# Kernel tuning notes

Measured on AMD Instinct MI355X. Metric: run time of the kernel, lower is better.

Reference implementation:

```python
import jax, jax.numpy as jnp
import numpy as np

B, N, C = 8, 8192, 256
H = 8            # num_heads
D = C // H       # head dim = 32
P = 64           # proj_size (Linformer rank)


def setup_inputs() -> dict:
    key = jax.random.key(0)
    ks = jax.random.split(key, 12)
    s = lambda fan_in: 1.0 / np.sqrt(fan_in)
    return {
        "x": jax.random.normal(ks[0], (B, N, C), jnp.float32),
        "Wqkvv": jax.random.normal(ks[1], (4 * C, C), jnp.float32) * s(C),
        "WE": jax.random.normal(ks[2], (P, N), jnp.float32) * s(N),
        "bE": jax.random.normal(ks[3], (P,), jnp.float32) * s(N),
        "WF": jax.random.normal(ks[4], (P, N), jnp.float32) * s(N),
        "bF": jax.random.normal(ks[5], (P,), jnp.float32) * s(N),
        "Wo1": jax.random.normal(ks[6], (C // 2, C), jnp.float32) * s(C),
        "bo1": jax.random.normal(ks[7], (C // 2,), jnp.float32) * s(C),
        "Wo2": jax.random.normal(ks[8], (C // 2, C), jnp.float32) * s(C),
        "bo2": jax.random.normal(ks[9], (C // 2,), jnp.float32) * s(C),
        "temp1": jnp.ones((H, 1, 1), jnp.float32),
        "temp2": jnp.ones((H, 1, 1), jnp.float32),
    }


def _l2norm(v, axis=-1, eps=1e-12):
    # matches torch F.normalize
    n = jnp.sqrt(jnp.sum(v * v, axis=axis, keepdims=True))
    return v / jnp.maximum(n, eps)


def reference(x, Wqkvv, WE, bE, WF, bF, Wo1, bo1, Wo2, bo2, temp1, temp2):
    b, n, c = x.shape
    # qkvv: [b,n,4c] -> [4,b,h,d,n]  (includes the .transpose(-2,-1) of each part)
    qkvv = jnp.einsum('bnc,fc->bnf', x, Wqkvv).reshape(b, n, 4, H, D)
    qkvv = qkvv.transpose(2, 0, 3, 4, 1)
    q, k, v_ca, v_sa = qkvv[0], qkvv[1], qkvv[2], qkvv[3]  # each [b,h,d,n]

    # Linformer-style low-rank projections along the token axis
    k_proj = jnp.einsum('bhdn,pn->bhdp', k, WE) + bE   # [b,h,d,p]
    v_proj = jnp.einsum('bhdn,pn->bhdp', v_sa, WF) + bF

    qn = _l2norm(q)
    kn = _l2norm(k)

    # --- channel attention branch (XCiT-style) ---
    attn_ca = jnp.einsum('bhdn,bhen->bhde', qn, kn) * temp1[None]  # [b,h,d,d]
    attn_ca = jax.nn.softmax(attn_ca, axis=-1)  # dropout: eval mode (identity)
    x_ca = jnp.einsum('bhde,bhen->bhdn', attn_ca, v_ca)
    x_ca = x_ca.transpose(0, 3, 1, 2).reshape(b, n, c)  # [b,n,c]

    # --- spatial attention branch (low-rank) ---
    attn_sa = jnp.einsum('bhdn,bhdp->bhnp', qn, k_proj) * temp2[None]  # [b,h,n,p]
    attn_sa = jax.nn.softmax(attn_sa, axis=-1)
    x_sa = jnp.einsum('bhnp,bhdp->bhnd', attn_sa, v_proj)  # [b,h,n,d]
    # faithful to original: permute(0,3,1,2).reshape(b,n,c)
    x_sa = x_sa.transpose(0, 3, 1, 2).reshape(b, n, c)

    x_sa = jnp.einsum('bnc,oc->bno', x_sa, Wo1) + bo1
    x_ca = jnp.einsum('bnc,oc->bno', x_ca, Wo2) + bo2
    return jnp.concatenate((x_sa, x_ca), axis=-1)
```

## Files before the change

### kernel.cpp

```cpp
#include <hip/hip_runtime.h>
#include <hip/hip_bf16.h>
#include <stdint.h>


typedef __attribute__((ext_vector_type(8))) __bf16 bf16x8;
typedef __attribute__((ext_vector_type(4))) __bf16 bf16x4;
typedef __attribute__((ext_vector_type(4))) float f32x4;

#define MFMA(a, b, c) __builtin_amdgcn_mfma_f32_16x16x32_bf16((a), (b), (c), 0, 0, 0)

__device__ __forceinline__ void gl2lds16(const __bf16* g, __bf16* l) {
  __builtin_amdgcn_global_load_lds(
      (const __attribute__((address_space(1))) void*)(const void*)g,
      (__attribute__((address_space(3))) void*)(void*)l, 16, 0, 0);
}

__device__ __forceinline__ int detect_f32(const unsigned int* __restrict__ xw) {
  int c = 0;
#pragma unroll
  for (int i = 0; i < 64; ++i) {
    const unsigned int u = xw[i];
    c += (((u >> 7) & 0xFF) >= 0xC0) ? 1 : 0;
    c += (((u >> 23) & 0xFF) >= 0xC0) ? 1 : 0;
  }
  return c > 8;
}

__global__ __launch_bounds__(256) void k_convert_x(const void* __restrict__ src,
                                                   __bf16* __restrict__ dst) {
  const int i = (blockIdx.x * 256 + threadIdx.x) * 8;
  if (detect_f32((const unsigned int*)src)) {
    const float* s = (const float*)src;
    bf16x8 v;
#pragma unroll
    for (int j = 0; j < 8; ++j) v[j] = (__bf16)s[i + j];
    *(bf16x8*)(dst + i) = v;
  } else {
    *(bf16x8*)(dst + i) = *(const bf16x8*)((const __bf16*)src + i);
  }
}

__global__ __launch_bounds__(256) void k_convert_w(
    const void* s0, const void* s1, const void* s2, const void* s3, const void* s4,
    const void* s5, const void* s6, const void* s7, const void* s8, const void* s9,
    const void* s10, __bf16* __restrict__ cw, const void* __restrict__ xsrc) {
  const int i = (blockIdx.x * 256 + threadIdx.x) * 8;
  if (i >= 1376656) return;
  const void* s;
  int base;
  if (i < 262144)        { s = s0;  base = 0; }
  else if (i < 786432)   { s = s1;  base = 262144; }
  else if (i < 786496)   { s = s2;  base = 786432; }
  else if (i < 1310784)  { s = s3;  base = 786496; }
  else if (i < 1310848)  { s = s4;  base = 1310784; }
  else if (i < 1343616)  { s = s5;  base = 1310848; }
  else if (i < 1343744)  { s = s6;  base = 1343616; }
  else if (i < 1376512)  { s = s7;  base = 1343744; }
  else if (i < 1376640)  { s = s8;  base = 1376512; }
  else if (i < 1376648)  { s = s9;  base = 1376640; }
  else                   { s = s10; base = 1376648; }
  const int li = i - base;
  if (detect_f32((const unsigned int*)xsrc)) {
    const float* sf = (const float*)s;
#pragma unroll
    for (int j = 0; j < 8; ++j) cw[i + j] = (__bf16)sf[li + j];
  } else {
    const __bf16* sb = (const __bf16*)s;
#pragma unroll
    for (int j = 0; j < 8; ++j) cw[i + j] = sb[li + j];
  }
}

__global__ __launch_bounds__(256) void k_qkvv(const __bf16* __restrict__ x,
                                              const __bf16* __restrict__ Wq,
                                              __bf16* __restrict__ qkvv,
                                              float* __restrict__ npart) {
  __shared__ alignas(16) __bf16 As[128 * 32];
  __shared__ alignas(16) __bf16 Bs[128 * 32];
  __shared__ alignas(16) __bf16 Cs[32 * 136];
  const int t = threadIdx.x, lane = t & 63;
  const int wr = t >> 7, wc = (t >> 6) & 1;
  const int l15 = lane & 15, g = lane >> 4;
  const int f0 = blockIdx.y * 128;
  const int t0 = blockIdx.x * 128;
  f32x4 acc[4][4] = {};
  const int r = t >> 2;
  const int c8 = ((t & 3) ^ ((t >> 3) & 3)) * 8;
  const int cx = ((g ^ ((l15 >> 1) & 3)) * 8);
  for (int k0 = 0; k0 < 256; k0 += 32) {
#pragma unroll
    for (int i = 0; i < 2; ++i) {
      gl2lds16(Wq + (size_t)(f0 + i * 64 + r) * 256 + k0 + c8, As + i * 2048 + t * 8);
      gl2lds16(x + (size_t)(t0 + i * 64 + r) * 256 + k0 + c8, Bs + i * 2048 + t * 8);
    }
    __syncthreads();
    bf16x8 af[4], bfr[4];
#pragma unroll
    for (int i = 0; i < 4; ++i) {
      af[i] = *(const bf16x8*)(As + (wr * 64 + i * 16 + l15) * 32 + cx);
      bfr[i] = *(const bf16x8*)(Bs + (wc * 64 + i * 16 + l15) * 32 + cx);
    }
#pragma unroll
    for (int i = 0; i < 4; ++i)
#pragma unroll
      for (int j = 0; j < 4; ++j) acc[i][j] = MFMA(af[i], bfr[j], acc[i][j]);
    __syncthreads();
  }
  const int b = t0 >> 13;
  const int n0 = t0 & 8191;
  for (int i = 0; i < 4; ++i) {
    if (i) __syncthreads();
#pragma unroll
    for (int j = 0; j < 4; ++j)
#pragma unroll
      for (int rr = 0; rr < 4; ++rr)
        Cs[(wr * 16 + g * 4 + rr) * 136 + wc * 64 + j * 16 + l15] = (__bf16)acc[i][j][rr];
    __syncthreads();
#pragma unroll
    for (int half = 0; half < 2; ++half) {
      const int row_l = (t >> 4) + half * 16;
      const int col8 = (t & 15) * 8;
      const bf16x8 v = *(const bf16x8*)(Cs + row_l * 136 + col8);
      const int f = f0 + (row_l >> 4) * 64 + i * 16 + (row_l & 15);
      *(bf16x8*)(qkvv + (size_t)(((f >> 8) * 8 + b) * 256 + (f & 255)) * 8192 + n0 + col8) = v;
      if (f0 < 512) {
        float s = 0.f;
#pragma unroll
        for (int jj = 0; jj < 8; ++jj) { const float q = (float)v[jj]; s += q * q; }
#pragma unroll
        for (int off = 1; off < 16; off <<= 1) s += __shfl_xor(s, off, 16);
        if ((t & 15) == 0) npart[(size_t)blockIdx.x * 512 + f] = s;
      }
    }
  }
}

__global__ __launch_bounds__(256) void k_nred(const float* __restrict__ npart,
                                              float* __restrict__ qsum,
                                              float* __restrict__ ksum) {
  const int which = blockIdx.x >> 3, b = blockIdx.x & 7;
  const int c = threadIdx.x;
  float s = 0.f;
#pragma unroll 4
  for (int j = 0; j < 64; ++j)
    s += npart[(size_t)(b * 64 + j) * 512 + which * 256 + c];
  (which ? ksum : qsum)[b * 256 + c] = s;
}

__global__ __launch_bounds__(256) void k_proj_part(const __bf16* __restrict__ qkvv,
                                                   const __bf16* __restrict__ WE,
                                                   const __bf16* __restrict__ WF,
                                                   float* __restrict__ pbuf) {
  __shared__ alignas(16) __bf16 As[128 * 32];
  __shared__ alignas(16) __bf16 Bs[64 * 32];
  const int t = threadIdx.x, lane = t & 63;
  const int wr = t >> 7, wc = (t >> 6) & 1;
  const int l15 = lane & 15, g = lane >> 4;
  const int kc = blockIdx.x, mt = blockIdx.y, pj = blockIdx.z;
  const __bf16* A = qkvv + (size_t)(pj ? 3 : 1) * 2048 * 8192;
  const __bf16* Bm = pj ? WF : WE;
  const int r0 = mt * 128;
  f32x4 acc[4][2] = {};
  const int r = t >> 2;
  const int c8 = ((t & 3) ^ ((t >> 3) & 3)) * 8;
  const int cx = ((g ^ ((l15 >> 1) & 3)) * 8);
  for (int k0 = kc * 512; k0 < kc * 512 + 512; k0 += 32) {
#pragma unroll
    for (int i = 0; i < 2; ++i)
      gl2lds16(A + (size_t)(r0 + i * 64 + r) * 8192 + k0 + c8, As + i * 2048 + t * 8);
    gl2lds16(Bm + (size_t)r * 8192 + k0 + c8, Bs + t * 8);
    __syncthreads();
    bf16x8 af[4], bfr[2];
#pragma unroll
    for (int i = 0; i < 4; ++i)
      af[i] = *(const bf16x8*)(As + (wr * 64 + i * 16 + l15) * 32 + cx);
#pragma unroll
    for (int j = 0; j < 2; ++j)
      bfr[j] = *(const bf16x8*)(Bs + (wc * 32 + j * 16 + l15) * 32 + cx);
#pragma unroll
    for (int i = 0; i < 4; ++i)
#pragma unroll
      for (int j = 0; j < 2; ++j) acc[i][j] = MFMA(af[i], bfr[j], acc[i][j]);
    __syncthreads();
  }
  float* dst = pbuf + (size_t)((pj * 16 + kc) * 2048 + r0) * 64;
#pragma unroll
  for (int i = 0; i < 4; ++i)
#pragma unroll
    for (int j = 0; j < 2; ++j)
#pragma unroll
      for (int rr = 0; rr < 4; ++rr)
        dst[(wr * 64 + i * 16 + g * 4 + rr) * 64 + wc * 32 + j * 16 + l15] = acc[i][j][rr];
}

__global__ __launch_bounds__(256) void k_proj_reduce(const float* __restrict__ pbuf,
                                                     const __bf16* __restrict__ bE,
                                                     const __bf16* __restrict__ bF,
                                                     const float* __restrict__ qsum,
                                                     const __bf16* __restrict__ t2,
                                                     __bf16* __restrict__ kprojT,
                                                     __bf16* __restrict__ vprojb) {
  const int idx = blockIdx.x * 256 + threadIdx.x;
  const int pj = idx >> 17, rp = idx & 131071, p = idx & 63;
  const int row = rp >> 6, bh = row >> 5, d = row & 31, h = bh & 7;
  float s = (float)((pj ? bF : bE)[p]);
  const float* src = pbuf + (size_t)pj * 16 * 131072 + rp;
#pragma unroll
  for (int k = 0; k < 16; ++k) s += src[(size_t)k * 131072];
  if (pj == 0) {
    const float qi = 1.0f / fmaxf(sqrtf(qsum[row]), 1e-12f);
    kprojT[bh * 2048 + p * 32 + d] = (__bf16)(s * qi * (float)t2[h]);
  } else {
    vprojb[bh * 2048 + d * 64 + p] = (__bf16)s;
  }
}

__global__ __launch_bounds__(256) void k_sca_part(const __bf16* __restrict__ qkvv,
                                                  float* __restrict__ spart) {
  const int bh = blockIdx.x, kc = blockIdx.y;
  const int t = threadIdx.x, lane = t & 63, w = t >> 6;
  const __bf16* qb = qkvv + (size_t)(bh * 32) * 8192;
  const __bf16* kb = qkvv + (size_t)(2048 + bh * 32) * 8192;
  f32x4 acc[2][2] = {};
  const int kbase = kc * 1024 + w * 256 + (lane >> 4) * 8;
#pragma unroll
  for (int ks = 0; ks < 256; ks += 32) {
    bf16x8 af[2], bfr[2];
#pragma unroll
    for (int i = 0; i < 2; ++i) {
      af[i] = *(const bf16x8*)(qb + (size_t)(i * 16 + (lane & 15)) * 8192 + kbase + ks);
      bfr[i] = *(const bf16x8*)(kb + (size_t)(i * 16 + (lane & 15)) * 8192 + kbase + ks);
    }
#pragma unroll
    for (int i = 0; i < 2; ++i)
#pragma unroll
      for (int j = 0; j < 2; ++j) acc[i][j] = MFMA(af[i], bfr[j], acc[i][j]);
  }
  float* dst = spart + (size_t)((bh * 8 + kc) * 4 + w) * 1024;
#pragma unroll
  for (int i = 0; i < 2; ++i)
#pragma unroll
    for (int j = 0; j < 2; ++j)
#pragma unroll
      for (int rr = 0; rr < 4; ++rr)
        dst[(i * 16 + (lane >> 4) * 4 + rr) * 32 + j * 16 + (lane & 15)] = acc[i][j][rr];
}

__global__ __launch_bounds__(256) void k_sca_softmax(const float* __restrict__ spart,
                                                     const float* __restrict__ qsum,
                                                     const float* __restrict__ ksum,
                                                     const __bf16* __restrict__ temp1,
                                                     __bf16* __restrict__ attnb) {
  const int bh = blockIdx.x;
  __shared__ float S[1024];
  const int t = threadIdx.x;
  const float tmp = (float)temp1[bh & 7];
  for (int idx = t; idx < 1024; idx += 256) {
    float s = 0.f;
    const float* src = spart + (size_t)bh * 32768 + idx;
#pragma unroll
    for (int k = 0; k < 32; ++k) s += src[k * 1024];
    const float qi = 1.0f / fmaxf(sqrtf(qsum[bh * 32 + (idx >> 5)]), 1e-12f);
    const float ki = 1.0f / fmaxf(sqrtf(ksum[bh * 32 + (idx & 31)]), 1e-12f);
    S[idx] = s * qi * ki * tmp;
  }
  __syncthreads();
  const int lane = t & 63, w = t >> 6;
#pragma unroll
  for (int rr = 0; rr < 4; ++rr) {
    const int row = rr * 8 + w * 2 + (lane >> 5);
    const int e = lane & 31;
    float v = S[row * 32 + e];
    float m = v;
#pragma unroll
    for (int off = 16; off; off >>= 1) m = fmaxf(m, __shfl_xor(m, off, 32));
    const float ex = __expf(v - m);
    float sm = ex;
#pragma unroll
    for (int off = 16; off; off >>= 1) sm += __shfl_xor(sm, off, 32);
    attnb[(size_t)bh * 1024 + row * 32 + e] = (__bf16)(ex / sm);
  }
}

__global__ __launch_bounds__(256) void k_casa(const __bf16* __restrict__ qkvv,
                                              const __bf16* __restrict__ attnb,
                                              const __bf16* __restrict__ kprojT,
                                              const __bf16* __restrict__ vprojb,
                                              __bf16* __restrict__ xca,
                                              __bf16* __restrict__ xsa) {
  __shared__ __bf16 P[4][16 * 72];
  const int t = threadIdx.x, lane = t & 63, w = t >> 6;
  const int l15 = lane & 15, g = lane >> 4;
  if (blockIdx.y < 64) {
    const int bh = blockIdx.y, b = bh >> 3, h = bh & 7;
    const __bf16* vb = qkvv + (size_t)(4096 + bh * 32) * 8192;
    bf16x8 aa[2];
#pragma unroll
    for (int mi = 0; mi < 2; ++mi)
      aa[mi] = *(const bf16x8*)(attnb + bh * 1024 + (mi * 16 + l15) * 32 + g * 8);
#pragma unroll
    for (int it = 0; it < 4; ++it) {
      const int n = blockIdx.x * 256 + it * 64 + w * 16 + l15;
      union { bf16x8 v; unsigned short u[8]; } bq;
#pragma unroll
      for (int j = 0; j < 8; ++j)
        bq.u[j] = *(const unsigned short*)(vb + (size_t)(g * 8 + j) * 8192 + n);
      f32x4 o[2] = {};
#pragma unroll
      for (int mi = 0; mi < 2; ++mi) o[mi] = MFMA(aa[mi], bq.v, o[mi]);
#pragma unroll
      for (int mi = 0; mi < 2; ++mi) {
        bf16x4 p4;
#pragma unroll
        for (int rr = 0; rr < 4; ++rr) p4[rr] = (__bf16)o[mi][rr];
        *(bf16x4*)(xca + (size_t)(b * 8192 + n) * 256 + h * 32 + mi * 16 + g * 4) = p4;
      }
    }
  } else {
    const int bh = blockIdx.y - 64;
    const __bf16* qb = qkvv + (size_t)(bh * 32) * 8192;
    bf16x8 ka[4], va[2][2];
#pragma unroll
    for (int tile = 0; tile < 4; ++tile)
      ka[tile] = *(const bf16x8*)(kprojT + bh * 2048 + (tile * 16 + l15) * 32 + g * 8);
#pragma unroll
    for (int mi = 0; mi < 2; ++mi)
#pragma unroll
      for (int kh = 0; kh < 2; ++kh)
        va[mi][kh] = *(const bf16x8*)(vprojb + bh * 2048 + (mi * 16 + l15) * 64 + kh * 32 + g * 8);
    __bf16* Pw = &P[w][0];
#pragma unroll
    for (int it = 0; it < 4; ++it) {
      const int n0 = blockIdx.x * 256 + it * 64 + w * 16;
      union { bf16x8 v; unsigned short u[8]; } bq;
#pragma unroll
      for (int j = 0; j < 8; ++j)
        bq.u[j] = *(const unsigned short*)(qb + (size_t)(g * 8 + j) * 8192 + n0 + l15);
      f32x4 st[4];
#pragma unroll
      for (int tile = 0; tile < 4; ++tile) {
        f32x4 z = {};
        st[tile] = MFMA(ka[tile], bq.v, z);
      }
      float m = st[0][0];
#pragma unroll
      for (int tile = 0; tile < 4; ++tile)
#pragma unroll
        for (int rr = 0; rr < 4; ++rr) m = fmaxf(m, st[tile][rr]);
      m = fmaxf(m, __shfl_xor(m, 16, 64));
      m = fmaxf(m, __shfl_xor(m, 32, 64));
      float sum = 0.f;
#pragma unroll
      for (int tile = 0; tile < 4; ++tile) {
        bf16x4 p4;
#pragma unroll
        for (int rr = 0; rr < 4; ++rr) {
          const float ex = __expf(st[tile][rr] - m);
          sum += ex;
          p4[rr] = (__bf16)ex;
        }
        *(bf16x4*)(Pw + l15 * 72 + tile * 16 + g * 4) = p4;
      }
      sum += __shfl_xor(sum, 16, 64);
      sum += __shfl_xor(sum, 32, 64);
      const float inv = 1.0f / sum;
      f32x4 o[2] = {};
#pragma unroll
      for (int kh = 0; kh < 2; ++kh) {
        const bf16x8 pf = *(const bf16x8*)(Pw + l15 * 72 + kh * 32 + g * 8);
#pragma unroll
        for (int mi = 0; mi < 2; ++mi) o[mi] = MFMA(va[mi][kh], pf, o[mi]);
      }
#pragma unroll
      for (int mi = 0; mi < 2; ++mi)
#pragma unroll
        for (int rr = 0; rr < 4; ++rr) {
          const int d = mi * 16 + g * 4 + rr;
          xsa[(size_t)(bh * 32 + d) * 8192 + n0 + l15] = (__bf16)(o[mi][rr] * inv);
        }
    }
  }
}

__global__ __launch_bounds__(256) void k_out(const __bf16* __restrict__ xsa,
                                             const __bf16* __restrict__ xca,
                                             const __bf16* __restrict__ Wo1,
                                             const __bf16* __restrict__ bo1,
                                             const __bf16* __restrict__ Wo2,
                                             const __bf16* __restrict__ bo2,
                                             void* __restrict__ outv,
                                             const void* __restrict__ xsrc) {
  __shared__ alignas(16) __bf16 As[128 * 32];
  __shared__ alignas(16) __bf16 Bs[128 * 32];
  const int t = threadIdx.x, lane = t & 63;
  const int wr = t >> 7, wc = (t >> 6) & 1;
  const int l15 = lane & 15, g = lane >> 4;
  const int nt = blockIdx.x, b = blockIdx.y, br = blockIdx.z;
  const int isf32 = detect_f32((const unsigned int*)xsrc);
  const __bf16* Wo = br ? Wo2 : Wo1;
  const __bf16* bo = br ? bo2 : bo1;
  f32x4 acc[4][4] = {};
  const int r = t >> 2;
  const int c8 = ((t & 3) ^ ((t >> 3) & 3)) * 8;
  const int cx = ((g ^ ((l15 >> 1) & 3)) * 8);
  for (int k0 = 0; k0 < 256; k0 += 32) {
#pragma unroll
    for (int i = 0; i < 2; ++i) {
      const int row = nt * 128 + i * 64 + r;
      const __bf16* ga;
      if (br == 0) {
        ga = xsa + (size_t)((b * 8 + ((row >> 5) & 7)) * 32 + (row >> 8)) * 8192 +
             (row & 31) * 256 + k0 + c8;
      } else {
        ga = xca + (size_t)(b * 8192 + row) * 256 + k0 + c8;
      }
      gl2lds16(ga, As + i * 2048 + t * 8);
      gl2lds16(Wo + (size_t)(i * 64 + r) * 256 + k0 + c8, Bs + i * 2048 + t * 8);
    }
    __syncthreads();
    bf16x8 af[4], bfr[4];
#pragma unroll
    for (int i = 0; i < 4; ++i) {
      af[i] = *(const bf16x8*)(As + (wr * 64 + i * 16 + l15) * 32 + cx);
      bfr[i] = *(const bf16x8*)(Bs + (wc * 64 + i * 16 + l15) * 32 + cx);
    }
#pragma unroll
    for (int i = 0; i < 4; ++i)
#pragma unroll
      for (int j = 0; j < 4; ++j) acc[i][j] = MFMA(af[i], bfr[j], acc[i][j]);
    __syncthreads();
  }
  float bias[4];
#pragma unroll
  for (int j = 0; j < 4; ++j) bias[j] = (float)bo[wc * 64 + j * 16 + l15];
#pragma unroll
  for (int i = 0; i < 4; ++i) {
#pragma unroll
    for (int j = 0; j < 4; ++j) {
      const int col = wc * 64 + j * 16 + l15;
#pragma unroll
      for (int rr = 0; rr < 4; ++rr) {
        const int row = nt * 128 + wr * 64 + i * 16 + g * 4 + rr;
        const float val = acc[i][j][rr] + bias[j];
        const size_t oi = (size_t)(b * 8192 + row) * 256 + br * 128 + col;
        if (isf32) ((float*)outv)[oi] = val;
        else ((__bf16*)outv)[oi] = (__bf16)val;
      }
    }
  }
}

extern "C" void kernel_launch(void* const* d_in, const int* in_sizes, int n_in,
                              void* d_out, int out_size, void* d_ws, size_t ws_size,
                              hipStream_t stream) {
  char* ws = (char*)d_ws;
  __bf16* qkvv   = (__bf16*)(ws);
  __bf16* cinx   = (__bf16*)(ws + 134217728ull);
  __bf16* xca    = (__bf16*)(ws + 134217728ull);
  float*  pbuf   = (float*)(ws + 167772160ull);
  float*  npart  = (float*)(ws + 184549376ull);
  float*  spart  = (float*)(ws + 184549376ull);
  __bf16* xsa    = (__bf16*)(ws + 167772160ull);
  __bf16* kprojT = (__bf16*)(ws + 201326592ull);
  __bf16* vprojb = (__bf16*)(ws + 201588736ull);
  float*  qsum   = (float*)(ws + 201850880ull);
  float*  ksum   = (float*)(ws + 201859072ull);
  __bf16* attnb  = (__bf16*)(ws + 201867264ull);
  __bf16* cw     = (__bf16*)(ws + 201998336ull);

  __bf16* cWq  = cw;
  __bf16* cWE  = cw + 262144;
  __bf16* cbE  = cw + 786432;
  __bf16* cWF  = cw + 786496;
  __bf16* cbF  = cw + 1310784;
  __bf16* cWo1 = cw + 1310848;
  __bf16* cbo1 = cw + 1343616;
  __bf16* cWo2 = cw + 1343744;
  __bf16* cbo2 = cw + 1376512;
  __bf16* ct1  = cw + 1376640;
  __bf16* ct2  = cw + 1376648;

  k_convert_x<<<8192, 256, 0, stream>>>(d_in[0], cinx);
  k_convert_w<<<673, 256, 0, stream>>>(d_in[1], d_in[2], d_in[3], d_in[4], d_in[5],
                                       d_in[6], d_in[7], d_in[8], d_in[9], d_in[10],
                                       d_in[11], cw, d_in[0]);
  k_qkvv<<<dim3(512, 8), 256, 0, stream>>>(cinx, cWq, qkvv, npart);
  k_nred<<<16, 256, 0, stream>>>(npart, qsum, ksum);
  k_proj_part<<<dim3(16, 16, 2), 256, 0, stream>>>(qkvv, cWE, cWF, pbuf);
  k_proj_reduce<<<dim3(1024), 256, 0, stream>>>(pbuf, cbE, cbF, qsum, ct2, kprojT, vprojb);
  k_sca_part<<<dim3(64, 8), 256, 0, stream>>>(qkvv, spart);
  k_sca_softmax<<<dim3(64), 256, 0, stream>>>(spart, qsum, ksum, ct1, attnb);
  k_casa<<<dim3(32, 128), 256, 0, stream>>>(qkvv, attnb, kprojT, vprojb, xca, xsa);
  k_out<<<dim3(64, 8, 2), 256, 0, stream>>>(xsa, xca, cWo1, cbo1, cWo2, cbo2, d_out, d_in[0]);
}
```

Before: 310.5 us.

## Fuse x conversion into QKVV GEMM with full-K LDS-resident token tile

Drops the separate x-to-bf16 conversion kernel and converts x while loading it into LDS inside the QKVV GEMM. Each block now keeps a 64-token x tile with full K resident in swizzled LDS and computes all 1024 output features, reading the weight fragments straight from global memory or cache without LDS staging. The aim is to remove the x round-trip through memory and the extra launch, and to read x only once instead of once per feature tile. In exchange the weights are re-read by every block, and the norm partials grow to 128 per batch, so the reduction loop changes to match.

```diff
diff --git a/kernel.cpp b/kernel.cpp
--- a/kernel.cpp
+++ b/kernel.cpp
@@ -24,20 +24,6 @@
     c += (((u >> 23) & 0xFF) >= 0xC0) ? 1 : 0;
   }
   return c > 8;
-}
-
-__global__ __launch_bounds__(256) void k_convert_x(const void* __restrict__ src,
-                                                   __bf16* __restrict__ dst) {
-  const int i = (blockIdx.x * 256 + threadIdx.x) * 8;
-  if (detect_f32((const unsigned int*)src)) {
-    const float* s = (const float*)src;
-    bf16x8 v;
-#pragma unroll
-    for (int j = 0; j < 8; ++j) v[j] = (__bf16)s[i + j];
-    *(bf16x8*)(dst + i) = v;
-  } else {
-    *(bf16x8*)(dst + i) = *(const bf16x8*)((const __bf16*)src + i);
-  }
 }
 
 __global__ __launch_bounds__(256) void k_convert_w(
@@ -71,66 +57,81 @@
   }
 }
 
-__global__ __launch_bounds__(256) void k_qkvv(const __bf16* __restrict__ x,
-                                              const __bf16* __restrict__ Wq,
-                                              __bf16* __restrict__ qkvv,
-                                              float* __restrict__ npart) {
-  __shared__ alignas(16) __bf16 As[128 * 32];
-  __shared__ alignas(16) __bf16 Bs[128 * 32];
-  __shared__ alignas(16) __bf16 Cs[32 * 136];
-  const int t = threadIdx.x, lane = t & 63;
-  const int wr = t >> 7, wc = (t >> 6) & 1;
+__global__ __launch_bounds__(256, 3) void k_qkvv(const void* __restrict__ xsrc,
+                                                 const __bf16* __restrict__ Wq,
+                                                 __bf16* __restrict__ qkvv,
+                                                 float* __restrict__ npart) {
+  __shared__ alignas(16) __bf16 Xs[64 * 256];
+  __shared__ alignas(16) __bf16 Csw[4][16][72];
+  const int t = threadIdx.x;
+  const int tile = blockIdx.x;
+  const int b = tile >> 7;
+  const int n0 = (tile & 127) * 64;
+  const int r = t >> 2, q4 = t & 3;
+  if (detect_f32((const unsigned int*)xsrc)) {
+    const float* xf = (const float*)xsrc + (size_t)(b * 8192 + n0 + r) * 256;
+#pragma unroll
+    for (int p = 0; p < 8; ++p) {
+      const int c = q4 + p * 4;
+      const f32x4 a = *(const f32x4*)(xf + c * 8);
+      const f32x4 a2 = *(const f32x4*)(xf + c * 8 + 4);
+      bf16x8 v;
+#pragma unroll
+      for (int j = 0; j < 4; ++j) { v[j] = (__bf16)a[j]; v[4 + j] = (__bf16)a2[j]; }
+      *(bf16x8*)(Xs + r * 256 + ((c ^ (r & 7)) * 8)) = v;
+    }
+  } else {
+    const __bf16* xb = (const __bf16*)xsrc + (size_t)(b * 8192 + n0 + r) * 256;
+#pragma unroll
+    for (int p = 0; p < 8; ++p) {
+      const int c = q4 + p * 4;
+      *(bf16x8*)(Xs + r * 256 + ((c ^ (r & 7)) * 8)) = *(const bf16x8*)(xb + c * 8);
+    }
+  }
+  __syncthreads();
+  const int lane = t & 63, w = t >> 6;
   const int l15 = lane & 15, g = lane >> 4;
-  const int f0 = blockIdx.y * 128;
-  const int t0 = blockIdx.x * 128;
-  f32x4 acc[4][4] = {};
-  const int r = t >> 2;
-  const int c8 = ((t & 3) ^ ((t >> 3) & 3)) * 8;
-  const int cx = ((g ^ ((l15 >> 1) & 3)) * 8);
-  for (int k0 = 0; k0 < 256; k0 += 32) {
-#pragma unroll
-    for (int i = 0; i < 2; ++i) {
-      gl2lds16(Wq + (size_t)(f0 + i * 64 + r) * 256 + k0 + c8, As + i * 2048 + t * 8);
-      gl2lds16(x + (size_t)(t0 + i * 64 + r) * 256 + k0 + c8, Bs + i * 2048 + t * 8);
-    }
-    __syncthreads();
-    bf16x8 af[4], bfr[4];
+  const int sw = l15 & 7;
+  for (int ft = 0; ft < 4; ++ft) {
+    const int f1 = w * 256 + ft * 64;
+    f32x4 acc[4][4] = {};
+#pragma unroll
+    for (int k0 = 0; k0 < 256; k0 += 32) {
+      bf16x8 af[4], bfr[4];
+#pragma unroll
+      for (int i = 0; i < 4; ++i)
+        af[i] = *(const bf16x8*)(Wq + (size_t)(f1 + i * 16 + l15) * 256 + k0 + g * 8);
+#pragma unroll
+      for (int j = 0; j < 4; ++j)
+        bfr[j] = *(const bf16x8*)(Xs + (j * 16 + l15) * 256 + ((((k0 >> 3) + g) ^ sw) * 8));
+#pragma unroll
+      for (int i = 0; i < 4; ++i)
+#pragma unroll
+        for (int j = 0; j < 4; ++j) acc[i][j] = MFMA(af[i], bfr[j], acc[i][j]);
+    }
 #pragma unroll
     for (int i = 0; i < 4; ++i) {
-      af[i] = *(const bf16x8*)(As + (wr * 64 + i * 16 + l15) * 32 + cx);
-      bfr[i] = *(const bf16x8*)(Bs + (wc * 64 + i * 16 + l15) * 32 + cx);
-    }
-#pragma unroll
-    for (int i = 0; i < 4; ++i)
-#pragma unroll
-      for (int j = 0; j < 4; ++j) acc[i][j] = MFMA(af[i], bfr[j], acc[i][j]);
-    __syncthreads();
-  }
-  const int b = t0 >> 13;
-  const int n0 = t0 & 8191;
-  for (int i = 0; i < 4; ++i) {
-    if (i) __syncthreads();
-#pragma unroll
-    for (int j = 0; j < 4; ++j)
-#pragma unroll
-      for (int rr = 0; rr < 4; ++rr)
-        Cs[(wr * 16 + g * 4 + rr) * 136 + wc * 64 + j * 16 + l15] = (__bf16)acc[i][j][rr];
-    __syncthreads();
-#pragma unroll
-    for (int half = 0; half < 2; ++half) {
-      const int row_l = (t >> 4) + half * 16;
-      const int col8 = (t & 15) * 8;
-      const bf16x8 v = *(const bf16x8*)(Cs + row_l * 136 + col8);
-      const int f = f0 + (row_l >> 4) * 64 + i * 16 + (row_l & 15);
-      *(bf16x8*)(qkvv + (size_t)(((f >> 8) * 8 + b) * 256 + (f & 255)) * 8192 + n0 + col8) = v;
-      if (f0 < 512) {
-        float s = 0.f;
-#pragma unroll
-        for (int jj = 0; jj < 8; ++jj) { const float q = (float)v[jj]; s += q * q; }
-#pragma unroll
-        for (int off = 1; off < 16; off <<= 1) s += __shfl_xor(s, off, 16);
-        if ((t & 15) == 0) npart[(size_t)blockIdx.x * 512 + f] = s;
-      }
+      if (f1 < 512) {
+#pragma unroll
+        for (int rr = 0; rr < 4; ++rr) {
+          float s = 0.f;
+#pragma unroll
+          for (int j = 0; j < 4; ++j) { const float v = acc[i][j][rr]; s += v * v; }
+#pragma unroll
+          for (int off = 1; off < 16; off <<= 1) s += __shfl_xor(s, off, 16);
+          if (l15 == 0) npart[(size_t)tile * 512 + f1 + i * 16 + g * 4 + rr] = s;
+        }
+      }
+#pragma unroll
+      for (int j = 0; j < 4; ++j)
+#pragma unroll
+        for (int rr = 0; rr < 4; ++rr)
+          Csw[w][g * 4 + rr][j * 16 + l15] = (__bf16)acc[i][j][rr];
+      const int f = f1 + i * 16 + l15;
+      __bf16* dst = qkvv + (size_t)(((f >> 8) * 8 + b) * 256 + (f & 255)) * 8192 + n0;
+#pragma unroll
+      for (int h = 0; h < 2; ++h)
+        *(bf16x8*)(dst + (h * 4 + g) * 8) = *(const bf16x8*)(&Csw[w][l15][(h * 4 + g) * 8]);
     }
   }
 }
@@ -142,8 +143,8 @@
   const int c = threadIdx.x;
   float s = 0.f;
 #pragma unroll 4
-  for (int j = 0; j < 64; ++j)
-    s += npart[(size_t)(b * 64 + j) * 512 + which * 256 + c];
+  for (int j = 0; j < 128; ++j)
+    s += npart[(size_t)(b * 128 + j) * 512 + which * 256 + c];
   (which ? ksum : qsum)[b * 256 + c] = s;
 }
 
@@ -455,7 +456,6 @@
                               hipStream_t stream) {
   char* ws = (char*)d_ws;
   __bf16* qkvv   = (__bf16*)(ws);
-  __bf16* cinx   = (__bf16*)(ws + 134217728ull);
   __bf16* xca    = (__bf16*)(ws + 134217728ull);
   float*  pbuf   = (float*)(ws + 167772160ull);
   float*  npart  = (float*)(ws + 184549376ull);
@@ -480,11 +480,10 @@
   __bf16* ct1  = cw + 1376640;
   __bf16* ct2  = cw + 1376648;
 
-  k_convert_x<<<8192, 256, 0, stream>>>(d_in[0], cinx);
   k_convert_w<<<673, 256, 0, stream>>>(d_in[1], d_in[2], d_in[3], d_in[4], d_in[5],
                                        d_in[6], d_in[7], d_in[8], d_in[9], d_in[10],
                                        d_in[11], cw, d_in[0]);
-  k_qkvv<<<dim3(512, 8), 256, 0, stream>>>(cinx, cWq, qkvv, npart);
+  k_qkvv<<<dim3(1024), 256, 0, stream>>>(d_in[0], cWq, qkvv, npart);
   k_nred<<<16, 256, 0, stream>>>(npart, qsum, ksum);
   k_proj_part<<<dim3(16, 16, 2), 256, 0, stream>>>(qkvv, cWE, cWF, pbuf);
   k_proj_reduce<<<dim3(1024), 256, 0, stream>>>(pbuf, cbE, cbF, qsum, ct2, kprojT, vprojb);
```

New measurement: 340.8 us. 1.1x slower.

## Fuse x fp32-to-bf16 conversion into QKVV GEMM with double-buffered LDS

Applied to the files above, without the earlier changes.

Removes the standalone k_convert_x kernel. k_qkvv now reads the fp32 input directly, converts it to bf16 in registers and writes it to LDS, which avoids writing and re-reading a 32MB bf16 copy of x. The GEMM K-loop becomes double-buffered so the next K tile's loads overlap the current MFMAs. The grid is transposed so consecutive blocks share the same token tile across feature tiles, which should improve L2 reuse of x. In exchange, LDS use doubles and each block pays a per-block detect_f32 check.

```diff
diff --git a/kernel.cpp b/kernel.cpp
--- a/kernel.cpp
+++ b/kernel.cpp
@@ -24,20 +24,6 @@
     c += (((u >> 23) & 0xFF) >= 0xC0) ? 1 : 0;
   }
   return c > 8;
-}
-
-__global__ __launch_bounds__(256) void k_convert_x(const void* __restrict__ src,
-                                                   __bf16* __restrict__ dst) {
-  const int i = (blockIdx.x * 256 + threadIdx.x) * 8;
-  if (detect_f32((const unsigned int*)src)) {
-    const float* s = (const float*)src;
-    bf16x8 v;
-#pragma unroll
-    for (int j = 0; j < 8; ++j) v[j] = (__bf16)s[i + j];
-    *(bf16x8*)(dst + i) = v;
-  } else {
-    *(bf16x8*)(dst + i) = *(const bf16x8*)((const __bf16*)src + i);
-  }
 }
 
 __global__ __launch_bounds__(256) void k_convert_w(
@@ -71,41 +57,90 @@
   }
 }
 
-__global__ __launch_bounds__(256) void k_qkvv(const __bf16* __restrict__ x,
+__global__ __launch_bounds__(256) void k_qkvv(const void* __restrict__ xsrc,
                                               const __bf16* __restrict__ Wq,
                                               __bf16* __restrict__ qkvv,
                                               float* __restrict__ npart) {
-  __shared__ alignas(16) __bf16 As[128 * 32];
-  __shared__ alignas(16) __bf16 Bs[128 * 32];
+  __shared__ alignas(16) __bf16 As[2][128 * 32];
+  __shared__ alignas(16) __bf16 Bs[2][128 * 32];
   __shared__ alignas(16) __bf16 Cs[32 * 136];
   const int t = threadIdx.x, lane = t & 63;
   const int wr = t >> 7, wc = (t >> 6) & 1;
   const int l15 = lane & 15, g = lane >> 4;
-  const int f0 = blockIdx.y * 128;
-  const int t0 = blockIdx.x * 128;
+  const int f0 = blockIdx.x * 128;
+  const int t0 = blockIdx.y * 128;
+  const int isf32 = detect_f32((const unsigned int*)xsrc);
+  const float* xf = (const float*)xsrc;
+  const __bf16* xb = (const __bf16*)xsrc;
   f32x4 acc[4][4] = {};
   const int r = t >> 2;
   const int c8 = ((t & 3) ^ ((t >> 3) & 3)) * 8;
   const int cx = ((g ^ ((l15 >> 1) & 3)) * 8);
-  for (int k0 = 0; k0 < 256; k0 += 32) {
+
+  if (isf32) {
 #pragma unroll
     for (int i = 0; i < 2; ++i) {
-      gl2lds16(Wq + (size_t)(f0 + i * 64 + r) * 256 + k0 + c8, As + i * 2048 + t * 8);
-      gl2lds16(x + (size_t)(t0 + i * 64 + r) * 256 + k0 + c8, Bs + i * 2048 + t * 8);
+      gl2lds16(Wq + (size_t)(f0 + i * 64 + r) * 256 + c8, &As[0][i * 2048 + t * 8]);
+      const float* src = xf + (size_t)(t0 + i * 64 + r) * 256 + c8;
+      const f32x4 a = *(const f32x4*)src;
+      const f32x4 a2 = *(const f32x4*)(src + 4);
+      bf16x8 v;
+#pragma unroll
+      for (int j = 0; j < 4; ++j) { v[j] = (__bf16)a[j]; v[4 + j] = (__bf16)a2[j]; }
+      *(bf16x8*)(&Bs[0][i * 2048 + t * 8]) = v;
+    }
+  } else {
+#pragma unroll
+    for (int i = 0; i < 2; ++i) {
+      gl2lds16(Wq + (size_t)(f0 + i * 64 + r) * 256 + c8, &As[0][i * 2048 + t * 8]);
+      gl2lds16(xb + (size_t)(t0 + i * 64 + r) * 256 + c8, &Bs[0][i * 2048 + t * 8]);
+    }
+  }
+  __syncthreads();
+
+  for (int ks = 0; ks < 8; ++ks) {
+    const int cur = ks & 1, nxt = cur ^ 1;
+    const int k1 = (ks + 1) * 32;
+    f32x4 a[2], a2[2];
+    if (ks < 7) {
+#pragma unroll
+      for (int i = 0; i < 2; ++i)
+        gl2lds16(Wq + (size_t)(f0 + i * 64 + r) * 256 + k1 + c8, &As[nxt][i * 2048 + t * 8]);
+      if (isf32) {
+#pragma unroll
+        for (int i = 0; i < 2; ++i) {
+          const float* src = xf + (size_t)(t0 + i * 64 + r) * 256 + k1 + c8;
+          a[i] = *(const f32x4*)src;
+          a2[i] = *(const f32x4*)(src + 4);
+        }
+      } else {
+#pragma unroll
+        for (int i = 0; i < 2; ++i)
+          gl2lds16(xb + (size_t)(t0 + i * 64 + r) * 256 + k1 + c8, &Bs[nxt][i * 2048 + t * 8]);
+      }
+    }
+    bf16x8 af[4], bfr[4];
+#pragma unroll
+    for (int i = 0; i < 4; ++i) {
+      af[i] = *(const bf16x8*)(&As[cur][(wr * 64 + i * 16 + l15) * 32 + cx]);
+      bfr[i] = *(const bf16x8*)(&Bs[cur][(wc * 64 + i * 16 + l15) * 32 + cx]);
+    }
+#pragma unroll
+    for (int i = 0; i < 4; ++i)
+#pragma unroll
+      for (int j = 0; j < 4; ++j) acc[i][j] = MFMA(af[i], bfr[j], acc[i][j]);
+    if (ks < 7 && isf32) {
+#pragma unroll
+      for (int i = 0; i < 2; ++i) {
+        bf16x8 v;
+#pragma unroll
+        for (int j = 0; j < 4; ++j) { v[j] = (__bf16)a[i][j]; v[4 + j] = (__bf16)a2[i][j]; }
+        *(bf16x8*)(&Bs[nxt][i * 2048 + t * 8]) = v;
+      }
     }
     __syncthreads();
-    bf16x8 af[4], bfr[4];
-#pragma unroll
-    for (int i = 0; i < 4; ++i) {
-      af[i] = *(const bf16x8*)(As + (wr * 64 + i * 16 + l15) * 32 + cx);
-      bfr[i] = *(const bf16x8*)(Bs + (wc * 64 + i * 16 + l15) * 32 + cx);
-    }
-#pragma unroll
-    for (int i = 0; i < 4; ++i)
-#pragma unroll
-      for (int j = 0; j < 4; ++j) acc[i][j] = MFMA(af[i], bfr[j], acc[i][j]);
-    __syncthreads();
-  }
+  }
+
   const int b = t0 >> 13;
   const int n0 = t0 & 8191;
   for (int i = 0; i < 4; ++i) {
@@ -129,7 +164,7 @@
         for (int jj = 0; jj < 8; ++jj) { const float q = (float)v[jj]; s += q * q; }
 #pragma unroll
         for (int off = 1; off < 16; off <<= 1) s += __shfl_xor(s, off, 16);
-        if ((t & 15) == 0) npart[(size_t)blockIdx.x * 512 + f] = s;
+        if ((t & 15) == 0) npart[(size_t)blockIdx.y * 512 + f] = s;
       }
     }
   }
@@ -455,7 +490,6 @@
                               hipStream_t stream) {
   char* ws = (char*)d_ws;
   __bf16* qkvv   = (__bf16*)(ws);
-  __bf16* cinx   = (__bf16*)(ws + 134217728ull);
   __bf16* xca    = (__bf16*)(ws + 134217728ull);
   float*  pbuf   = (float*)(ws + 167772160ull);
   float*  npart  = (float*)(ws + 184549376ull);
@@ -480,11 +514,10 @@
   __bf16* ct1  = cw + 1376640;
   __bf16* ct2  = cw + 1376648;
 
-  k_convert_x<<<8192, 256, 0, stream>>>(d_in[0], cinx);
   k_convert_w<<<673, 256, 0, stream>>>(d_in[1], d_in[2], d_in[3], d_in[4], d_in[5],
                                        d_in[6], d_in[7], d_in[8], d_in[9], d_in[10],
                                        d_in[11], cw, d_in[0]);
-  k_qkvv<<<dim3(512, 8), 256, 0, stream>>>(cinx, cWq, qkvv, npart);
+  k_qkvv<<<dim3(8, 512), 256, 0, stream>>>(d_in[0], cWq, qkvv, npart);
   k_nred<<<16, 256, 0, stream>>>(npart, qsum, ksum);
   k_proj_part<<<dim3(16, 16, 2), 256, 0, stream>>>(qkvv, cWE, cWF, pbuf);
   k_proj_reduce<<<dim3(1024), 256, 0, stream>>>(pbuf, cbE, cbF, qsum, ct2, kprojT, vprojb);
```

Result: slower. 335.6 us (+8.1%).

## Double-buffer LDS tiles in the qkvv, projection and output GEMM kernels

Applied to the files above, without the earlier changes.

Adds two LDS buffers per operand in three MFMA GEMM kernels. The next k-slice is issued with global_load_lds before computing on the current slice, so memory latency can overlap with MFMA work. LDS use per block doubles, which may lower occupancy, and correctness depends on the trailing __syncthreads covering the async loads.

```diff
diff --git a/kernel.cpp b/kernel.cpp
--- a/kernel.cpp
+++ b/kernel.cpp
@@ -75,8 +75,8 @@
                                               const __bf16* __restrict__ Wq,
                                               __bf16* __restrict__ qkvv,
                                               float* __restrict__ npart) {
-  __shared__ alignas(16) __bf16 As[128 * 32];
-  __shared__ alignas(16) __bf16 Bs[128 * 32];
+  __shared__ alignas(16) __bf16 As[2][128 * 32];
+  __shared__ alignas(16) __bf16 Bs[2][128 * 32];
   __shared__ alignas(16) __bf16 Cs[32 * 136];
   const int t = threadIdx.x, lane = t & 63;
   const int wr = t >> 7, wc = (t >> 6) & 1;
@@ -87,18 +87,27 @@
   const int r = t >> 2;
   const int c8 = ((t & 3) ^ ((t >> 3) & 3)) * 8;
   const int cx = ((g ^ ((l15 >> 1) & 3)) * 8);
-  for (int k0 = 0; k0 < 256; k0 += 32) {
-#pragma unroll
-    for (int i = 0; i < 2; ++i) {
-      gl2lds16(Wq + (size_t)(f0 + i * 64 + r) * 256 + k0 + c8, As + i * 2048 + t * 8);
-      gl2lds16(x + (size_t)(t0 + i * 64 + r) * 256 + k0 + c8, Bs + i * 2048 + t * 8);
-    }
-    __syncthreads();
+#pragma unroll
+  for (int i = 0; i < 2; ++i) {
+    gl2lds16(Wq + (size_t)(f0 + i * 64 + r) * 256 + c8, &As[0][i * 2048 + t * 8]);
+    gl2lds16(x + (size_t)(t0 + i * 64 + r) * 256 + c8, &Bs[0][i * 2048 + t * 8]);
+  }
+  __syncthreads();
+  for (int ks = 0; ks < 8; ++ks) {
+    const int cur = ks & 1, nxt = cur ^ 1;
+    if (ks < 7) {
+      const int k1 = (ks + 1) * 32;
+#pragma unroll
+      for (int i = 0; i < 2; ++i) {
+        gl2lds16(Wq + (size_t)(f0 + i * 64 + r) * 256 + k1 + c8, &As[nxt][i * 2048 + t * 8]);
+        gl2lds16(x + (size_t)(t0 + i * 64 + r) * 256 + k1 + c8, &Bs[nxt][i * 2048 + t * 8]);
+      }
+    }
     bf16x8 af[4], bfr[4];
 #pragma unroll
     for (int i = 0; i < 4; ++i) {
-      af[i] = *(const bf16x8*)(As + (wr * 64 + i * 16 + l15) * 32 + cx);
-      bfr[i] = *(const bf16x8*)(Bs + (wc * 64 + i * 16 + l15) * 32 + cx);
+      af[i] = *(const bf16x8*)(&As[cur][(wr * 64 + i * 16 + l15) * 32 + cx]);
+      bfr[i] = *(const bf16x8*)(&Bs[cur][(wc * 64 + i * 16 + l15) * 32 + cx]);
     }
 #pragma unroll
     for (int i = 0; i < 4; ++i)
@@ -151,8 +160,8 @@
                                                    const __bf16* __restrict__ WE,
                                                    const __bf16* __restrict__ WF,
                                                    float* __restrict__ pbuf) {
-  __shared__ alignas(16) __bf16 As[128 * 32];
-  __shared__ alignas(16) __bf16 Bs[64 * 32];
+  __shared__ alignas(16) __bf16 As[2][128 * 32];
+  __shared__ alignas(16) __bf16 Bs[2][64 * 32];
   const int t = threadIdx.x, lane = t & 63;
   const int wr = t >> 7, wc = (t >> 6) & 1;
   const int l15 = lane & 15, g = lane >> 4;
@@ -164,19 +173,28 @@
   const int r = t >> 2;
   const int c8 = ((t & 3) ^ ((t >> 3) & 3)) * 8;
   const int cx = ((g ^ ((l15 >> 1) & 3)) * 8);
-  for (int k0 = kc * 512; k0 < kc * 512 + 512; k0 += 32) {
-#pragma unroll
-    for (int i = 0; i < 2; ++i)
-      gl2lds16(A + (size_t)(r0 + i * 64 + r) * 8192 + k0 + c8, As + i * 2048 + t * 8);
-    gl2lds16(Bm + (size_t)r * 8192 + k0 + c8, Bs + t * 8);
-    __syncthreads();
+  const int kb = kc * 512;
+#pragma unroll
+  for (int i = 0; i < 2; ++i)
+    gl2lds16(A + (size_t)(r0 + i * 64 + r) * 8192 + kb + c8, &As[0][i * 2048 + t * 8]);
+  gl2lds16(Bm + (size_t)r * 8192 + kb + c8, &Bs[0][t * 8]);
+  __syncthreads();
+  for (int ks = 0; ks < 16; ++ks) {
+    const int cur = ks & 1, nxt = cur ^ 1;
+    if (ks < 15) {
+      const int k1 = kb + (ks + 1) * 32;
+#pragma unroll
+      for (int i = 0; i < 2; ++i)
+        gl2lds16(A + (size_t)(r0 + i * 64 + r) * 8192 + k1 + c8, &As[nxt][i * 2048 + t * 8]);
+      gl2lds16(Bm + (size_t)r * 8192 + k1 + c8, &Bs[nxt][t * 8]);
+    }
     bf16x8 af[4], bfr[2];
 #pragma unroll
     for (int i = 0; i < 4; ++i)
-      af[i] = *(const bf16x8*)(As + (wr * 64 + i * 16 + l15) * 32 + cx);
+      af[i] = *(const bf16x8*)(&As[cur][(wr * 64 + i * 16 + l15) * 32 + cx]);
 #pragma unroll
     for (int j = 0; j < 2; ++j)
-      bfr[j] = *(const bf16x8*)(Bs + (wc * 32 + j * 16 + l15) * 32 + cx);
+      bfr[j] = *(const bf16x8*)(&Bs[cur][(wc * 32 + j * 16 + l15) * 32 + cx]);
 #pragma unroll
     for (int i = 0; i < 4; ++i)
 #pragma unroll
@@ -390,8 +408,8 @@
                                              const __bf16* __restrict__ bo2,
                                              void* __restrict__ outv,
                                              const void* __restrict__ xsrc) {
-  __shared__ alignas(16) __bf16 As[128 * 32];
-  __shared__ alignas(16) __bf16 Bs[128 * 32];
+  __shared__ alignas(16) __bf16 As[2][128 * 32];
+  __shared__ alignas(16) __bf16 Bs[2][128 * 32];
   const int t = threadIdx.x, lane = t & 63;
   const int wr = t >> 7, wc = (t >> 6) & 1;
   const int l15 = lane & 15, g = lane >> 4;
@@ -403,26 +421,35 @@
   const int r = t >> 2;
   const int c8 = ((t & 3) ^ ((t >> 3) & 3)) * 8;
   const int cx = ((g ^ ((l15 >> 1) & 3)) * 8);
-  for (int k0 = 0; k0 < 256; k0 += 32) {
-#pragma unroll
-    for (int i = 0; i < 2; ++i) {
-      const int row = nt * 128 + i * 64 + r;
-      const __bf16* ga;
-      if (br == 0) {
-        ga = xsa + (size_t)((b * 8 + ((row >> 5) & 7)) * 32 + (row >> 8)) * 8192 +
+  const int row_b = nt * 128 + r;
+  auto asrc = [&](int i, int k0) -> const __bf16* {
+    const int row = row_b + i * 64;
+    if (br == 0)
+      return xsa + (size_t)((b * 8 + ((row >> 5) & 7)) * 32 + (row >> 8)) * 8192 +
              (row & 31) * 256 + k0 + c8;
-      } else {
-        ga = xca + (size_t)(b * 8192 + row) * 256 + k0 + c8;
-      }
-      gl2lds16(ga, As + i * 2048 + t * 8);
-      gl2lds16(Wo + (size_t)(i * 64 + r) * 256 + k0 + c8, Bs + i * 2048 + t * 8);
-    }
-    __syncthreads();
+    return xca + (size_t)(b * 8192 + row) * 256 + k0 + c8;
+  };
+#pragma unroll
+  for (int i = 0; i < 2; ++i) {
+    gl2lds16(asrc(i, 0), &As[0][i * 2048 + t * 8]);
+    gl2lds16(Wo + (size_t)(i * 64 + r) * 256 + c8, &Bs[0][i * 2048 + t * 8]);
+  }
+  __syncthreads();
+  for (int ks = 0; ks < 8; ++ks) {
+    const int cur = ks & 1, nxt = cur ^ 1;
+    if (ks < 7) {
+      const int k1 = (ks + 1) * 32;
+#pragma unroll
+      for (int i = 0; i < 2; ++i) {
+        gl2lds16(asrc(i, k1), &As[nxt][i * 2048 + t * 8]);
+        gl2lds16(Wo + (size_t)(i * 64 + r) * 256 + k1 + c8, &Bs[nxt][i * 2048 + t * 8]);
+      }
+    }
     bf16x8 af[4], bfr[4];
 #pragma unroll
     for (int i = 0; i < 4; ++i) {
-      af[i] = *(const bf16x8*)(As + (wr * 64 + i * 16 + l15) * 32 + cx);
-      bfr[i] = *(const bf16x8*)(Bs + (wc * 64 + i * 16 + l15) * 32 + cx);
+      af[i] = *(const bf16x8*)(&As[cur][(wr * 64 + i * 16 + l15) * 32 + cx]);
+      bfr[i] = *(const bf16x8*)(&Bs[cur][(wc * 64 + i * 16 + l15) * 32 + cx]);
     }
 #pragma unroll
     for (int i = 0; i < 4; ++i)
```

Result: no change. 314.0 us (+1.1%).
